# Kernel optimization log

Measured on AMD Instinct MI355X. Metric: run time of the kernel, lower is better.

## Reference

```python
import jax, jax.numpy as jnp
import numpy as np

NU, NI, D, E = 50000, 100000, 128, 500000
UMAX, IMAX = 50, 50
SQRT_D = float(np.sqrt(D))


def seg_softmax(vals, seg, n):
    # numerically stable softmax over edges grouped by segment id (sparse row softmax)
    m = jax.ops.segment_max(vals, seg, num_segments=n)
    ex = jnp.exp(vals - m[seg])
    s = jax.ops.segment_sum(ex, seg, num_segments=n)
    return ex / s[seg]


def setup_inputs() -> dict:
    key = jax.random.key(0)
    ks = jax.random.split(key, 20)
    w = lambda k: jax.random.normal(k, (D, D), dtype=jnp.float32) * 0.05
    return {
        "u_emb": jax.random.normal(ks[0], (NU, D), dtype=jnp.float32),
        "i_emb": jax.random.normal(ks[1], (NI, D), dtype=jnp.float32),
        "edge_u": jax.random.randint(ks[2], (E,), 0, NU),
        "edge_i": jax.random.randint(ks[3], (E,), 0, NI),
        "rui": jax.random.randint(ks[4], (E,), 0, UMAX),
        "riu": jax.random.randint(ks[5], (E,), 0, IMAX),
        "last_u_items": jax.random.randint(ks[6], (NU,), 0, NI),
        "last_i_users": jax.random.randint(ks[7], (NU,), 0, NU),
        "W1": w(ks[8]), "W2": w(ks[9]), "W1b": w(ks[10]), "W2b": w(ks[11]),
        "W3": w(ks[12]), "W4": w(ks[13]),
        "pV": jax.random.normal(ks[14], (UMAX, D), dtype=jnp.float32),
        "pK": jax.random.normal(ks[15], (IMAX, D), dtype=jnp.float32),
        "last_user_table": jax.random.normal(ks[16], (NU, D), dtype=jnp.float32),
        "last_item_table": jax.random.normal(ks[17], (NI, D), dtype=jnp.float32),
    }


def reference(u_emb, i_emb, edge_u, edge_i, rui, riu, last_u_items, last_i_users,
              W1, W2, W1b, W2b, W3, W4, pV, pK, last_user_table, last_item_table):
    # nn.Linear: y = x @ W.T
    um = u_emb @ W2.T            # (NU, D) user messages
    im = i_emb @ W1.T            # (NI, D) item messages
    um_e = um[edge_u]            # (E, D) gathered per edge
    im_e = im[edge_i]            # (E, D)

    # ---- long term ----
    # dense e = um @ im.T masked to edges == per-edge dot products (same math)
    e_vals = jnp.sum(um_e * im_e, axis=-1)                     # (E,)
    pVui = pV[rui]                                             # (E, D)
    pKiu = pK[riu]                                             # (E, D)
    e_ui = e_vals + jnp.sum(um_e * pVui, axis=-1)
    e_iu = e_vals + jnp.sum(im_e * pKiu, axis=-1)
    alphas = seg_softmax(e_ui / SQRT_D, edge_u, NU)            # softmax over items per user
    betas = seg_softmax(e_iu / SQRT_D, edge_i, NI)             # softmax over users per item

    umb = u_emb @ W2b.T
    imb = i_emb @ W1b.T
    # pass_messages: out[row] = sum_e alpha_e * (messages[col_e] + p_e)
    hLu = jax.ops.segment_sum(alphas[:, None] * (imb[edge_i] + pKiu), edge_u, num_segments=NU)
    hLi = jax.ops.segment_sum(betas[:, None] * (umb[edge_u] + pVui), edge_i, num_segments=NI)

    # ---- short term ----
    li = last_item_table[last_u_items] @ W3.T                  # (NU, D)
    lu = last_user_table[last_i_users] @ W4.T                  # (NU, D)
    a_vals = jnp.sum(li[edge_u] * im_e, axis=-1)               # (E,)
    b_vals = jnp.sum(lu[edge_u] * im_e, axis=-1)               # (E,)
    alphas_s = seg_softmax(a_vals / SQRT_D, edge_u, NU)
    betas_s = seg_softmax(b_vals / SQRT_D, edge_i, NI)
    # p = ones -> messages + 1
    hSu = jax.ops.segment_sum(alphas_s[:, None] * (im_e + 1.0), edge_u, num_segments=NU)
    hSi = jax.ops.segment_sum(betas_s[:, None] * (um_e + 1.0), edge_i, num_segments=NI)

    return (hLu, hSu, hLi, hSi)
```

## Files before the change

kernel.cpp:

```cpp
#include <hip/hip_runtime.h>
#include <hip/hip_bf16.h>
#include <math.h>

#define D_ 128
#define INV_SQRT_D 0.08838834764831845f
#define SCAN_CH 16
#define SCAN_TILE (256 * SCAN_CH)

typedef __bf16 bf16x8 __attribute__((ext_vector_type(8)));
typedef __bf16 bf16x4 __attribute__((ext_vector_type(4)));
typedef float f32x4 __attribute__((ext_vector_type(4)));

struct W6 { const float* p[6]; };

__device__ __forceinline__ void unpack8(bf16x8 v, float* f) {
    const uint32_t* u = (const uint32_t*)&v;
#pragma unroll
    for (int i = 0; i < 4; i++) {
        uint32_t w = u[i];
        f[2 * i]     = __uint_as_float(w << 16);
        f[2 * i + 1] = __uint_as_float(w & 0xffff0000u);
    }
}

__device__ __forceinline__ void unpack4(bf16x4 v, float* f) {
    const uint32_t* u = (const uint32_t*)&v;
#pragma unroll
    for (int i = 0; i < 2; i++) {
        uint32_t w = u[i];
        f[2 * i]     = __uint_as_float(w << 16);
        f[2 * i + 1] = __uint_as_float(w & 0xffff0000u);
    }
}

__global__ __launch_bounds__(256) void cvt_weights(W6 w, __bf16* __restrict__ out) {
    int idx = blockIdx.x * 256 + threadIdx.x;
    if (idx >= 6 * 16384) return;
    out[idx] = (__bf16)w.p[idx >> 14][idx & 16383];
}

__global__ __launch_bounds__(256) void cvt2(const float* __restrict__ a, const float* __restrict__ b,
                                            __bf16* __restrict__ oa, __bf16* __restrict__ ob, int n) {
    int idx = blockIdx.x * 256 + threadIdx.x;
    if (idx < n) { oa[idx] = (__bf16)a[idx]; ob[idx] = (__bf16)b[idx]; }
}

__global__ __launch_bounds__(256) void gemm_xwt(const float* __restrict__ X,
                                                const int* __restrict__ gidx,
                                                const __bf16* __restrict__ Wb,
                                                __bf16* __restrict__ Y, int rows) {
    int lane = threadIdx.x & 63;
    int wave = threadIdx.x >> 6;
    int row0 = blockIdx.x * 64 + wave * 16;
    if (row0 >= rows) return;
    int l16 = lane & 15, kh = lane >> 4;
    int ar = row0 + l16;
    int arc = ar < rows ? ar : rows - 1;
    long srcrow = gidx ? (long)gidx[arc] : (long)arc;
    const float* arow = X + (size_t)srcrow * D_;

    f32x4 acc[8] = {};
#pragma unroll
    for (int k0 = 0; k0 < D_; k0 += 32) {
        int kk = k0 + kh * 8;
        float4 a0 = *(const float4*)(arow + kk);
        float4 a1 = *(const float4*)(arow + kk + 4);
        bf16x8 af;
        af[0] = (__bf16)a0.x; af[1] = (__bf16)a0.y; af[2] = (__bf16)a0.z; af[3] = (__bf16)a0.w;
        af[4] = (__bf16)a1.x; af[5] = (__bf16)a1.y; af[6] = (__bf16)a1.z; af[7] = (__bf16)a1.w;
#pragma unroll
        for (int cb = 0; cb < 8; cb++) {
            bf16x8 bf = *(const bf16x8*)(Wb + (size_t)(cb * 16 + l16) * D_ + kk);
            acc[cb] = __builtin_amdgcn_mfma_f32_16x16x32_bf16(af, bf, acc[cb], 0, 0, 0);
        }
    }
#pragma unroll
    for (int cb = 0; cb < 8; cb++) {
#pragma unroll
        for (int j = 0; j < 4; j++) {
            int r = row0 + kh * 4 + j;
            if (r < rows) Y[(size_t)r * D_ + cb * 16 + l16] = (__bf16)acc[cb][j];
        }
    }
}

__global__ __launch_bounds__(256) void gemm_dual(const float* __restrict__ X,
                                                 const __bf16* __restrict__ WA,
                                                 const __bf16* __restrict__ WB,
                                                 __bf16* __restrict__ YA,
                                                 __bf16* __restrict__ YB, int rows) {
    int lane = threadIdx.x & 63;
    int wave = threadIdx.x >> 6;
    int row0 = blockIdx.x * 64 + wave * 16;
    if (row0 >= rows) return;
    int l16 = lane & 15, kh = lane >> 4;
    int ar = row0 + l16;
    int arc = ar < rows ? ar : rows - 1;
    const float* arow = X + (size_t)arc * D_;

    f32x4 accA[8] = {}, accB[8] = {};
#pragma unroll
    for (int k0 = 0; k0 < D_; k0 += 32) {
        int kk = k0 + kh * 8;
        float4 a0 = *(const float4*)(arow + kk);
        float4 a1 = *(const float4*)(arow + kk + 4);
        bf16x8 af;
        af[0] = (__bf16)a0.x; af[1] = (__bf16)a0.y; af[2] = (__bf16)a0.z; af[3] = (__bf16)a0.w;
        af[4] = (__bf16)a1.x; af[5] = (__bf16)a1.y; af[6] = (__bf16)a1.z; af[7] = (__bf16)a1.w;
#pragma unroll
        for (int cb = 0; cb < 8; cb++) {
            bf16x8 bfA = *(const bf16x8*)(WA + (size_t)(cb * 16 + l16) * D_ + kk);
            accA[cb] = __builtin_amdgcn_mfma_f32_16x16x32_bf16(af, bfA, accA[cb], 0, 0, 0);
            bf16x8 bfB = *(const bf16x8*)(WB + (size_t)(cb * 16 + l16) * D_ + kk);
            accB[cb] = __builtin_amdgcn_mfma_f32_16x16x32_bf16(af, bfB, accB[cb], 0, 0, 0);
        }
    }
#pragma unroll
    for (int cb = 0; cb < 8; cb++) {
#pragma unroll
        for (int j = 0; j < 4; j++) {
            int r = row0 + kh * 4 + j;
            if (r < rows) {
                YA[(size_t)r * D_ + cb * 16 + l16] = (__bf16)accA[cb][j];
                YB[(size_t)r * D_ + cb * 16 + l16] = (__bf16)accB[cb][j];
            }
        }
    }
}

__global__ __launch_bounds__(256) void gemm_pvk(const __bf16* __restrict__ Xb,
                                                const __bf16* __restrict__ Pb,
                                                float* __restrict__ Y, int rows, int ncols) {
    int lane = threadIdx.x & 63;
    int wave = threadIdx.x >> 6;
    int row0 = blockIdx.x * 64 + wave * 16;
    if (row0 >= rows) return;
    int l16 = lane & 15, kh = lane >> 4;
    int ar = row0 + l16;
    int arc = ar < rows ? ar : rows - 1;
    const __bf16* arow = Xb + (size_t)arc * D_;

    f32x4 acc[4] = {};
#pragma unroll
    for (int k0 = 0; k0 < D_; k0 += 32) {
        int kk = k0 + kh * 8;
        bf16x8 af = *(const bf16x8*)(arow + kk);
#pragma unroll
        for (int cb = 0; cb < 4; cb++) {
            int br = cb * 16 + l16;
            if (br >= ncols) br = ncols - 1;
            bf16x8 bf = *(const bf16x8*)(Pb + (size_t)br * D_ + kk);
            acc[cb] = __builtin_amdgcn_mfma_f32_16x16x32_bf16(af, bf, acc[cb], 0, 0, 0);
        }
    }
#pragma unroll
    for (int cb = 0; cb < 4; cb++) {
        int col = cb * 16 + l16;
        if (col >= ncols) continue;
#pragma unroll
        for (int j = 0; j < 4; j++) {
            int r = row0 + kh * 4 + j;
            if (r < rows) Y[(size_t)r * ncols + col] = acc[cb][j];
        }
    }
}

__global__ __launch_bounds__(256) void hist2(const int* __restrict__ eu, const int* __restrict__ ei,
                                             int* __restrict__ cnt_all, int nu, int E) {
    int e = blockIdx.x * 256 + threadIdx.x;
    if (e < E) {
        atomicAdd(&cnt_all[eu[e]], 1);
        atomicAdd(&cnt_all[nu + ei[e]], 1);
    }
}

__global__ __launch_bounds__(256) void scan_phaseA(const int* __restrict__ cnt, int* __restrict__ part, int n) {
    __shared__ int wsum[4];
    int t = threadIdx.x, lane = t & 63, w = t >> 6;
    int i0 = blockIdx.x * SCAN_TILE + t * SCAN_CH;
    int tot = 0;
#pragma unroll
    for (int j = 0; j < SCAN_CH; j++) tot += (i0 + j < n) ? cnt[i0 + j] : 0;
#pragma unroll
    for (int d = 32; d; d >>= 1) tot += __shfl_xor(tot, d);
    if (lane == 0) wsum[w] = tot;
    __syncthreads();
    if (t == 0) part[blockIdx.x] = wsum[0] + wsum[1] + wsum[2] + wsum[3];
}

__global__ __launch_bounds__(1024) void scan_phaseB(int* __restrict__ part, int nb,
                                                    int* __restrict__ off, int n) {
    __shared__ int wsum[16];
    int t = threadIdx.x, lane = t & 63, w = t >> 6;
    int v = (t < nb) ? part[t] : 0;
    int x = v;
#pragma unroll
    for (int d = 1; d < 64; d <<= 1) {
        int y = __shfl_up(x, d);
        if (lane >= d) x += y;
    }
    if (lane == 63) wsum[w] = x;
    __syncthreads();
    int wbase = 0;
    for (int ww = 0; ww < w; ww++) wbase += wsum[ww];
    if (t < nb) part[t] = wbase + x - v;
    if (t == 1023) off[n] = wbase + x;
}

__global__ __launch_bounds__(256) void scan_phaseC(const int* __restrict__ cnt, const int* __restrict__ part,
                                                   int* __restrict__ off, int* __restrict__ pos, int n) {
    __shared__ int wsum[4];
    int t = threadIdx.x, lane = t & 63, w = t >> 6;
    int i0 = blockIdx.x * SCAN_TILE + t * SCAN_CH;
    int loc[SCAN_CH];
    int tot = 0;
#pragma unroll
    for (int j = 0; j < SCAN_CH; j++) {
        int v = (i0 + j < n) ? cnt[i0 + j] : 0;
        loc[j] = tot; tot += v;
    }
    int x = tot;
#pragma unroll
    for (int d = 1; d < 64; d <<= 1) {
        int y = __shfl_up(x, d);
        if (lane >= d) x += y;
    }
    if (lane == 63) wsum[w] = x;
    __syncthreads();
    int wbase = 0;
    for (int ww = 0; ww < w; ww++) wbase += wsum[ww];
    int excl = part[blockIdx.x] + wbase + x - tot;
#pragma unroll
    for (int j = 0; j < SCAN_CH; j++) {
        if (i0 + j < n) { off[i0 + j] = excl + loc[j]; pos[i0 + j] = excl + loc[j]; }
    }
}

__global__ __launch_bounds__(256) void scatter2(const int* __restrict__ eu, const int* __restrict__ ei,
                                                int* __restrict__ pos_all, int* __restrict__ list_all,
                                                int nu, int E) {
    int e = blockIdx.x * 256 + threadIdx.x;
    if (e < E) {
        int pu = atomicAdd(&pos_all[eu[e]], 1);
        list_all[pu] = e;
        int pi = atomicAdd(&pos_all[nu + ei[e]], 1);
        list_all[pi] = e;
    }
}

__global__ __launch_bounds__(256) void edge_dots16(const __bf16* __restrict__ um, const __bf16* __restrict__ im,
                                                   const __bf16* __restrict__ li, const __bf16* __restrict__ lu,
                                                   const float* __restrict__ upv, const float* __restrict__ ipk,
                                                   const int* __restrict__ eu, const int* __restrict__ ei,
                                                   const int* __restrict__ rui, const int* __restrict__ riu,
                                                   float* __restrict__ e_ui, float* __restrict__ e_iu,
                                                   float* __restrict__ a_log, float* __restrict__ b_log,
                                                   int E, int umax, int imax) {
    int wave = threadIdx.x >> 6;
    int lane = threadIdx.x & 63;
    int g = lane >> 4, l16 = lane & 15;
    int e = blockIdx.x * 16 + wave * 4 + g;
    if (e >= E) return;
    int u = eu[e], it = ei[e];
    bf16x8 umv = ((const bf16x8*)(um + (size_t)u * D_))[l16];
    bf16x8 imv = ((const bf16x8*)(im + (size_t)it * D_))[l16];
    bf16x8 liv = ((const bf16x8*)(li + (size_t)u * D_))[l16];
    bf16x8 luv = ((const bf16x8*)(lu + (size_t)u * D_))[l16];
    float fu[8], fi[8], fl[8], fg[8];
    unpack8(umv, fu); unpack8(imv, fi); unpack8(liv, fl); unpack8(luv, fg);
    float s_mm = 0.f, s_li = 0.f, s_lu = 0.f;
#pragma unroll
    for (int j = 0; j < 8; j++) {
        s_mm = fmaf(fu[j], fi[j], s_mm);
        s_li = fmaf(fl[j], fi[j], s_li);
        s_lu = fmaf(fg[j], fi[j], s_lu);
    }
#pragma unroll
    for (int d = 1; d < 16; d <<= 1) {
        s_mm += __shfl_xor(s_mm, d);
        s_li += __shfl_xor(s_li, d);
        s_lu += __shfl_xor(s_lu, d);
    }
    if (l16 == 0) {
        float uv = upv[(size_t)u * umax + rui[e]];
        float iv = ipk[(size_t)it * imax + riu[e]];
        e_ui[e]  = (s_mm + uv) * INV_SQRT_D;
        e_iu[e]  = (s_mm + iv) * INV_SQRT_D;
        a_log[e] = s_li * INV_SQRT_D;
        b_log[e] = s_lu * INV_SQRT_D;
    }
}

__global__ __launch_bounds__(256) void user_messages(const int* __restrict__ off_all, const int* __restrict__ list_all,
                                                     const int* __restrict__ ei, const int* __restrict__ riu,
                                                     const float* __restrict__ e_ui, const float* __restrict__ a_log,
                                                     const __bf16* __restrict__ imb, const __bf16* __restrict__ im,
                                                     const __bf16* __restrict__ pKb,
                                                     float* __restrict__ hLu, float* __restrict__ hSu, int nu) {
    int u = blockIdx.x * 4 + (threadIdx.x >> 6);
    if (u >= nu) return;
    int lane = threadIdx.x & 63;
    int g = lane >> 5, l32 = lane & 31;
    int off = off_all[u], n = off_all[u + 1] - off;
    float a1[4] = {}, a2[4] = {};
    float s1 = 0.f, s2 = 0.f;
    float m1 = -INFINITY, m2 = -INFINITY;
    for (int i = lane; i < n; i += 64) {
        int e = list_all[off + i];
        m1 = fmaxf(m1, e_ui[e]);
        m2 = fmaxf(m2, a_log[e]);
    }
#pragma unroll
    for (int d = 32; d; d >>= 1) {
        m1 = fmaxf(m1, __shfl_xor(m1, d));
        m2 = fmaxf(m2, __shfl_xor(m2, d));
    }
    for (int i = g; i < n; i += 2) {
        int e = list_all[off + i];
        float w1 = __expf(e_ui[e] - m1);
        float w2 = __expf(a_log[e] - m2);
        int item = ei[e];
        bf16x4 vb = ((const bf16x4*)(imb + (size_t)item * D_))[l32];
        bf16x4 vi = ((const bf16x4*)(im + (size_t)item * D_))[l32];
        bf16x4 pk = ((const bf16x4*)(pKb + (size_t)riu[e] * D_))[l32];
        float fb[4], fv[4], fp[4];
        unpack4(vb, fb); unpack4(vi, fv); unpack4(pk, fp);
        s1 += w1; s2 += w2;
#pragma unroll
        for (int j = 0; j < 4; j++) {
            a1[j] = fmaf(w1, fb[j] + fp[j], a1[j]);
            a2[j] = fmaf(w2, fv[j] + 1.f, a2[j]);
        }
    }
#pragma unroll
    for (int j = 0; j < 4; j++) {
        a1[j] += __shfl_xor(a1[j], 32);
        a2[j] += __shfl_xor(a2[j], 32);
    }
    s1 += __shfl_xor(s1, 32);
    s2 += __shfl_xor(s2, 32);
    float inv1 = n > 0 ? 1.f / s1 : 0.f;
    float inv2 = n > 0 ? 1.f / s2 : 0.f;
    if (lane < 32) {
        float4 o1 = make_float4(a1[0] * inv1, a1[1] * inv1, a1[2] * inv1, a1[3] * inv1);
        float4 o2 = make_float4(a2[0] * inv2, a2[1] * inv2, a2[2] * inv2, a2[3] * inv2);
        ((float4*)(hLu + (size_t)u * D_))[lane] = o1;
        ((float4*)(hSu + (size_t)u * D_))[lane] = o2;
    }
}

__global__ __launch_bounds__(256) void item_messages(const int* __restrict__ off_all, const int* __restrict__ list_all,
                                                     const int* __restrict__ eu, const int* __restrict__ rui,
                                                     const float* __restrict__ e_iu, const float* __restrict__ b_log,
                                                     const __bf16* __restrict__ umb, const __bf16* __restrict__ um,
                                                     const __bf16* __restrict__ pVb,
                                                     float* __restrict__ hLi, float* __restrict__ hSi,
                                                     int nu, int ni) {
    int it = blockIdx.x * 4 + (threadIdx.x >> 6);
    if (it >= ni) return;
    int lane = threadIdx.x & 63;
    int g = lane >> 5, l32 = lane & 31;
    int off = off_all[nu + it], n = off_all[nu + it + 1] - off;
    float a1[4] = {}, a2[4] = {};
    float s1 = 0.f, s2 = 0.f;
    float m1 = -INFINITY, m2 = -INFINITY;
    for (int i = lane; i < n; i += 64) {
        int e = list_all[off + i];
        m1 = fmaxf(m1, e_iu[e]);
        m2 = fmaxf(m2, b_log[e]);
    }
#pragma unroll
    for (int d = 32; d; d >>= 1) {
        m1 = fmaxf(m1, __shfl_xor(m1, d));
        m2 = fmaxf(m2, __shfl_xor(m2, d));
    }
    for (int i = g; i < n; i += 2) {
        int e = list_all[off + i];
        float w1 = __expf(e_iu[e] - m1);
        float w2 = __expf(b_log[e] - m2);
        int user = eu[e];
        bf16x4 vb = ((const bf16x4*)(umb + (size_t)user * D_))[l32];
        bf16x4 vu = ((const bf16x4*)(um + (size_t)user * D_))[l32];
        bf16x4 pv = ((const bf16x4*)(pVb + (size_t)rui[e] * D_))[l32];
        float fb[4], fv[4], fp[4];
        unpack4(vb, fb); unpack4(vu, fv); unpack4(pv, fp);
        s1 += w1; s2 += w2;
#pragma unroll
        for (int j = 0; j < 4; j++) {
            a1[j] = fmaf(w1, fb[j] + fp[j], a1[j]);
            a2[j] = fmaf(w2, fv[j] + 1.f, a2[j]);
        }
    }
#pragma unroll
    for (int j = 0; j < 4; j++) {
        a1[j] += __shfl_xor(a1[j], 32);
        a2[j] += __shfl_xor(a2[j], 32);
    }
    s1 += __shfl_xor(s1, 32);
    s2 += __shfl_xor(s2, 32);
    float inv1 = n > 0 ? 1.f / s1 : 0.f;
    float inv2 = n > 0 ? 1.f / s2 : 0.f;
    if (lane < 32) {
        float4 o1 = make_float4(a1[0] * inv1, a1[1] * inv1, a1[2] * inv1, a1[3] * inv1);
        float4 o2 = make_float4(a2[0] * inv2, a2[1] * inv2, a2[2] * inv2, a2[3] * inv2);
        ((float4*)(hLi + (size_t)it * D_))[lane] = o1;
        ((float4*)(hSi + (size_t)it * D_))[lane] = o2;
    }
}

extern "C" void kernel_launch(void* const* d_in, const int* in_sizes, int n_in,
                              void* d_out, int out_size, void* d_ws, size_t ws_size,
                              hipStream_t stream) {
    (void)n_in; (void)out_size; (void)ws_size;
    const float* u_emb = (const float*)d_in[0];
    const float* i_emb = (const float*)d_in[1];
    const int* edge_u = (const int*)d_in[2];
    const int* edge_i = (const int*)d_in[3];
    const int* rui = (const int*)d_in[4];
    const int* riu = (const int*)d_in[5];
    const int* last_u_items = (const int*)d_in[6];
    const int* last_i_users = (const int*)d_in[7];
    const float* W1  = (const float*)d_in[8];
    const float* W2  = (const float*)d_in[9];
    const float* W1b = (const float*)d_in[10];
    const float* W2b = (const float*)d_in[11];
    const float* W3  = (const float*)d_in[12];
    const float* W4  = (const float*)d_in[13];
    const float* pV  = (const float*)d_in[14];
    const float* pK  = (const float*)d_in[15];
    const float* last_user_table = (const float*)d_in[16];
    const float* last_item_table = (const float*)d_in[17];

    const int NU = in_sizes[0] / D_;
    const int NI = in_sizes[1] / D_;
    const int E  = in_sizes[2];
    const int UMAXr = in_sizes[14] / D_;
    const int IMAXr = in_sizes[15] / D_;
    const int NSEG = NU + NI;

    size_t cur = 0;
    auto alloc = [&](size_t bytes) -> void* {
        void* p = (char*)d_ws + cur;
        cur += (bytes + 255) & ~(size_t)255;
        return p;
    };

    __bf16* Wb     = (__bf16*)alloc(6 * 16384 * sizeof(__bf16));
    __bf16* pVb    = (__bf16*)alloc((size_t)UMAXr * D_ * 2);
    __bf16* pKb    = (__bf16*)alloc((size_t)IMAXr * D_ * 2);
    __bf16* um_bf  = (__bf16*)alloc((size_t)NU * D_ * 2);
    __bf16* umb_bf = (__bf16*)alloc((size_t)NU * D_ * 2);
    __bf16* li_bf  = (__bf16*)alloc((size_t)NU * D_ * 2);
    __bf16* lu_bf  = (__bf16*)alloc((size_t)NU * D_ * 2);
    __bf16* im_bf  = (__bf16*)alloc((size_t)NI * D_ * 2);
    __bf16* imb_bf = (__bf16*)alloc((size_t)NI * D_ * 2);
    float* upv   = (float*)alloc((size_t)NU * UMAXr * 4);
    float* ipk   = (float*)alloc((size_t)NI * IMAXr * 4);
    float* e_ui  = (float*)alloc((size_t)E * 4);
    float* e_iu  = (float*)alloc((size_t)E * 4);
    float* a_log = (float*)alloc((size_t)E * 4);
    float* b_log = (float*)alloc((size_t)E * 4);
    int* cnt_all  = (int*)alloc((size_t)NSEG * 4);
    int* off_all  = (int*)alloc((size_t)(NSEG + 1) * 4);
    int* pos_all  = (int*)alloc((size_t)NSEG * 4);
    int* list_all = (int*)alloc((size_t)2 * E * 4);
    int* parts    = (int*)alloc(1024 * 4);

    float* out = (float*)d_out;
    float* hLu = out;
    float* hSu = out + (size_t)NU * D_;
    float* hLi = out + (size_t)2 * NU * D_;
    float* hSi = out + (size_t)2 * NU * D_ + (size_t)NI * D_;

    W6 w6;
    w6.p[0] = W1; w6.p[1] = W2; w6.p[2] = W1b; w6.p[3] = W2b; w6.p[4] = W3; w6.p[5] = W4;
    cvt_weights<<<(6 * 16384 + 255) / 256, 256, 0, stream>>>(w6, Wb);
    cvt2<<<(UMAXr * D_ + 255) / 256, 256, 0, stream>>>(pV, pK, pVb, pKb, UMAXr * D_);

    hipMemsetAsync(cnt_all, 0, (size_t)NSEG * 4, stream);
    hist2<<<(E + 255) / 256, 256, 0, stream>>>(edge_u, edge_i, cnt_all, NU, E);
    int nb = (NSEG + SCAN_TILE - 1) / SCAN_TILE;
    scan_phaseA<<<nb, 256, 0, stream>>>(cnt_all, parts, NSEG);
    scan_phaseB<<<1, 1024, 0, stream>>>(parts, nb, off_all, NSEG);
    scan_phaseC<<<nb, 256, 0, stream>>>(cnt_all, parts, off_all, pos_all, NSEG);
    scatter2<<<(E + 255) / 256, 256, 0, stream>>>(edge_u, edge_i, pos_all, list_all, NU, E);

    int gu = (NU + 63) / 64, gi = (NI + 63) / 64;
    gemm_dual<<<gi, 256, 0, stream>>>(i_emb, Wb + 0 * 16384, Wb + 2 * 16384, im_bf, imb_bf, NI);
    gemm_dual<<<gu, 256, 0, stream>>>(u_emb, Wb + 1 * 16384, Wb + 3 * 16384, um_bf, umb_bf, NU);
    gemm_xwt<<<gu, 256, 0, stream>>>(last_item_table, last_u_items, Wb + 4 * 16384, li_bf, NU);
    gemm_xwt<<<gu, 256, 0, stream>>>(last_user_table, last_i_users, Wb + 5 * 16384, lu_bf, NU);

    gemm_pvk<<<gu, 256, 0, stream>>>(um_bf, pVb, upv, NU, UMAXr);
    gemm_pvk<<<gi, 256, 0, stream>>>(im_bf, pKb, ipk, NI, IMAXr);

    edge_dots16<<<(E + 15) / 16, 256, 0, stream>>>(um_bf, im_bf, li_bf, lu_bf, upv, ipk,
                                                   edge_u, edge_i, rui, riu,
                                                   e_ui, e_iu, a_log, b_log, E, UMAXr, IMAXr);

    user_messages<<<(NU + 3) / 4, 256, 0, stream>>>(off_all, list_all, edge_i, riu, e_ui, a_log,
                                                    imb_bf, im_bf, pKb, hLu, hSu, NU);
    item_messages<<<(NI + 3) / 4, 256, 0, stream>>>(off_all, list_all, edge_u, rui, e_iu, b_log,
                                                    umb_bf, um_bf, pVb, hLi, hSi, NU, NI);
}
```

Baseline: 576.9 us.

## Fuse edge logits into segment kernels with online softmax and interleaved row records

Removes the separate per-edge dot-product kernel and its four E-sized logit arrays. The user and item aggregation kernels now compute the logits themselves and use an online (running-max) softmax in a single pass over each segment. Projected embeddings are stored interleaved per row (im|imb, um|umb|lu), so the gathers for one edge hit contiguous memory. The cost is that each edge's dot products are recomputed on both the user side and the item side, plus extra exp and rescale work per edge in the online softmax.

```diff
diff --git a/kernel.cpp b/kernel.cpp
--- a/kernel.cpp
+++ b/kernel.cpp
@@ -13,16 +13,6 @@
 
 struct W6 { const float* p[6]; };
 
-__device__ __forceinline__ void unpack8(bf16x8 v, float* f) {
-    const uint32_t* u = (const uint32_t*)&v;
-#pragma unroll
-    for (int i = 0; i < 4; i++) {
-        uint32_t w = u[i];
-        f[2 * i]     = __uint_as_float(w << 16);
-        f[2 * i + 1] = __uint_as_float(w & 0xffff0000u);
-    }
-}
-
 __device__ __forceinline__ void unpack4(bf16x4 v, float* f) {
     const uint32_t* u = (const uint32_t*)&v;
 #pragma unroll
@@ -48,7 +38,7 @@
 __global__ __launch_bounds__(256) void gemm_xwt(const float* __restrict__ X,
                                                 const int* __restrict__ gidx,
                                                 const __bf16* __restrict__ Wb,
-                                                __bf16* __restrict__ Y, int rows) {
+                                                __bf16* __restrict__ Y, int ystride, int rows) {
     int lane = threadIdx.x & 63;
     int wave = threadIdx.x >> 6;
     int row0 = blockIdx.x * 64 + wave * 16;
@@ -79,7 +69,7 @@
 #pragma unroll
         for (int j = 0; j < 4; j++) {
             int r = row0 + kh * 4 + j;
-            if (r < rows) Y[(size_t)r * D_ + cb * 16 + l16] = (__bf16)acc[cb][j];
+            if (r < rows) Y[(size_t)r * ystride + cb * 16 + l16] = (__bf16)acc[cb][j];
         }
     }
 }
@@ -87,8 +77,8 @@
 __global__ __launch_bounds__(256) void gemm_dual(const float* __restrict__ X,
                                                  const __bf16* __restrict__ WA,
                                                  const __bf16* __restrict__ WB,
-                                                 __bf16* __restrict__ YA,
-                                                 __bf16* __restrict__ YB, int rows) {
+                                                 __bf16* __restrict__ YA, int sA,
+                                                 __bf16* __restrict__ YB, int sB, int rows) {
     int lane = threadIdx.x & 63;
     int wave = threadIdx.x >> 6;
     int row0 = blockIdx.x * 64 + wave * 16;
@@ -121,14 +111,14 @@
         for (int j = 0; j < 4; j++) {
             int r = row0 + kh * 4 + j;
             if (r < rows) {
-                YA[(size_t)r * D_ + cb * 16 + l16] = (__bf16)accA[cb][j];
-                YB[(size_t)r * D_ + cb * 16 + l16] = (__bf16)accB[cb][j];
+                YA[(size_t)r * sA + cb * 16 + l16] = (__bf16)accA[cb][j];
+                YB[(size_t)r * sB + cb * 16 + l16] = (__bf16)accB[cb][j];
             }
         }
     }
 }
 
-__global__ __launch_bounds__(256) void gemm_pvk(const __bf16* __restrict__ Xb,
+__global__ __launch_bounds__(256) void gemm_pvk(const __bf16* __restrict__ Xb, int xstride,
                                                 const __bf16* __restrict__ Pb,
                                                 float* __restrict__ Y, int rows, int ncols) {
     int lane = threadIdx.x & 63;
@@ -138,7 +128,7 @@
     int l16 = lane & 15, kh = lane >> 4;
     int ar = row0 + l16;
     int arc = ar < rows ? ar : rows - 1;
-    const __bf16* arow = Xb + (size_t)arc * D_;
+    const __bf16* arow = Xb + (size_t)arc * xstride;
 
     f32x4 acc[4] = {};
 #pragma unroll
@@ -248,163 +238,184 @@
     }
 }
 
-__global__ __launch_bounds__(256) void edge_dots16(const __bf16* __restrict__ um, const __bf16* __restrict__ im,
-                                                   const __bf16* __restrict__ li, const __bf16* __restrict__ lu,
-                                                   const float* __restrict__ upv, const float* __restrict__ ipk,
-                                                   const int* __restrict__ eu, const int* __restrict__ ei,
-                                                   const int* __restrict__ rui, const int* __restrict__ riu,
-                                                   float* __restrict__ e_ui, float* __restrict__ e_iu,
-                                                   float* __restrict__ a_log, float* __restrict__ b_log,
-                                                   int E, int umax, int imax) {
-    int wave = threadIdx.x >> 6;
-    int lane = threadIdx.x & 63;
-    int g = lane >> 4, l16 = lane & 15;
-    int e = blockIdx.x * 16 + wave * 4 + g;
-    if (e >= E) return;
-    int u = eu[e], it = ei[e];
-    bf16x8 umv = ((const bf16x8*)(um + (size_t)u * D_))[l16];
-    bf16x8 imv = ((const bf16x8*)(im + (size_t)it * D_))[l16];
-    bf16x8 liv = ((const bf16x8*)(li + (size_t)u * D_))[l16];
-    bf16x8 luv = ((const bf16x8*)(lu + (size_t)u * D_))[l16];
-    float fu[8], fi[8], fl[8], fg[8];
-    unpack8(umv, fu); unpack8(imv, fi); unpack8(liv, fl); unpack8(luv, fg);
-    float s_mm = 0.f, s_li = 0.f, s_lu = 0.f;
-#pragma unroll
-    for (int j = 0; j < 8; j++) {
-        s_mm = fmaf(fu[j], fi[j], s_mm);
-        s_li = fmaf(fl[j], fi[j], s_li);
-        s_lu = fmaf(fg[j], fi[j], s_lu);
-    }
-#pragma unroll
-    for (int d = 1; d < 16; d <<= 1) {
-        s_mm += __shfl_xor(s_mm, d);
-        s_li += __shfl_xor(s_li, d);
-        s_lu += __shfl_xor(s_lu, d);
-    }
-    if (l16 == 0) {
-        float uv = upv[(size_t)u * umax + rui[e]];
-        float iv = ipk[(size_t)it * imax + riu[e]];
-        e_ui[e]  = (s_mm + uv) * INV_SQRT_D;
-        e_iu[e]  = (s_mm + iv) * INV_SQRT_D;
-        a_log[e] = s_li * INV_SQRT_D;
-        b_log[e] = s_lu * INV_SQRT_D;
-    }
-}
-
-__global__ __launch_bounds__(256) void user_messages(const int* __restrict__ off_all, const int* __restrict__ list_all,
-                                                     const int* __restrict__ ei, const int* __restrict__ riu,
-                                                     const float* __restrict__ e_ui, const float* __restrict__ a_log,
-                                                     const __bf16* __restrict__ imb, const __bf16* __restrict__ im,
-                                                     const __bf16* __restrict__ pKb,
-                                                     float* __restrict__ hLu, float* __restrict__ hSu, int nu) {
+__global__ __launch_bounds__(256) void user_fused(const int* __restrict__ off_all, const int* __restrict__ list_all,
+                                                  const int* __restrict__ ei, const int* __restrict__ rui,
+                                                  const int* __restrict__ riu,
+                                                  const __bf16* __restrict__ i_rec,
+                                                  const __bf16* __restrict__ u_rec,
+                                                  const __bf16* __restrict__ li,
+                                                  const __bf16* __restrict__ pKb,
+                                                  const float* __restrict__ upv,
+                                                  float* __restrict__ hLu, float* __restrict__ hSu,
+                                                  int nu, int umax) {
     int u = blockIdx.x * 4 + (threadIdx.x >> 6);
     if (u >= nu) return;
     int lane = threadIdx.x & 63;
     int g = lane >> 5, l32 = lane & 31;
     int off = off_all[u], n = off_all[u + 1] - off;
-    float a1[4] = {}, a2[4] = {};
-    float s1 = 0.f, s2 = 0.f;
-    float m1 = -INFINITY, m2 = -INFINITY;
-    for (int i = lane; i < n; i += 64) {
-        int e = list_all[off + i];
-        m1 = fmaxf(m1, e_ui[e]);
-        m2 = fmaxf(m2, a_log[e]);
-    }
-#pragma unroll
-    for (int d = 32; d; d >>= 1) {
-        m1 = fmaxf(m1, __shfl_xor(m1, d));
-        m2 = fmaxf(m2, __shfl_xor(m2, d));
-    }
+    if (n == 0) {
+        if (lane < 32) {
+            ((float4*)(hLu + (size_t)u * D_))[l32] = make_float4(0.f, 0.f, 0.f, 0.f);
+            ((float4*)(hSu + (size_t)u * D_))[l32] = make_float4(0.f, 0.f, 0.f, 0.f);
+        }
+        return;
+    }
+    float um4[4], li4[4];
+    unpack4(*(const bf16x4*)(u_rec + (size_t)u * 384 + l32 * 4), um4);
+    unpack4(*(const bf16x4*)(li + (size_t)u * D_ + l32 * 4), li4);
+    const float* upv_row = upv + (size_t)u * umax;
+
+    float m1 = -INFINITY, s1 = 0.f, a1[4] = {};
+    float m2 = -INFINITY, s2 = 0.f, a2[4] = {};
     for (int i = g; i < n; i += 2) {
         int e = list_all[off + i];
-        float w1 = __expf(e_ui[e] - m1);
-        float w2 = __expf(a_log[e] - m2);
         int item = ei[e];
-        bf16x4 vb = ((const bf16x4*)(imb + (size_t)item * D_))[l32];
-        bf16x4 vi = ((const bf16x4*)(im + (size_t)item * D_))[l32];
-        bf16x4 pk = ((const bf16x4*)(pKb + (size_t)riu[e] * D_))[l32];
-        float fb[4], fv[4], fp[4];
-        unpack4(vb, fb); unpack4(vi, fv); unpack4(pk, fp);
-        s1 += w1; s2 += w2;
+        const __bf16* ib = i_rec + (size_t)item * 256;
+        bf16x4 imv  = ((const bf16x4*)ib)[l32];
+        bf16x4 imbv = ((const bf16x4*)(ib + 128))[l32];
+        bf16x4 pkv  = ((const bf16x4*)(pKb + (size_t)riu[e] * D_))[l32];
+        float uv = upv_row[rui[e]];
+        float fim[4], fimb[4], fpk[4];
+        unpack4(imv, fim); unpack4(imbv, fimb); unpack4(pkv, fpk);
+        float d1 = 0.f, d2 = 0.f;
 #pragma unroll
         for (int j = 0; j < 4; j++) {
-            a1[j] = fmaf(w1, fb[j] + fp[j], a1[j]);
-            a2[j] = fmaf(w2, fv[j] + 1.f, a2[j]);
-        }
-    }
-#pragma unroll
-    for (int j = 0; j < 4; j++) {
-        a1[j] += __shfl_xor(a1[j], 32);
-        a2[j] += __shfl_xor(a2[j], 32);
-    }
+            d1 = fmaf(um4[j], fim[j], d1);
+            d2 = fmaf(li4[j], fim[j], d2);
+        }
+#pragma unroll
+        for (int d = 16; d; d >>= 1) {
+            d1 += __shfl_xor(d1, d);
+            d2 += __shfl_xor(d2, d);
+        }
+        float lg1 = (d1 + uv) * INV_SQRT_D;
+        float lg2 = d2 * INV_SQRT_D;
+        float mn = fmaxf(m1, lg1);
+        float r  = __expf(m1 - mn);
+        float w  = __expf(lg1 - mn);
+        s1 = s1 * r + w; m1 = mn;
+#pragma unroll
+        for (int j = 0; j < 4; j++) a1[j] = fmaf(a1[j], r, w * (fimb[j] + fpk[j]));
+        mn = fmaxf(m2, lg2);
+        r  = __expf(m2 - mn);
+        w  = __expf(lg2 - mn);
+        s2 = s2 * r + w; m2 = mn;
+#pragma unroll
+        for (int j = 0; j < 4; j++) a2[j] = fmaf(a2[j], r, w * (fim[j] + 1.f));
+    }
+    float mo = __shfl_xor(m1, 32);
+    float mm = fmaxf(m1, mo);
+    float r  = __expf(m1 - mm);
+    s1 *= r;
+#pragma unroll
+    for (int j = 0; j < 4; j++) a1[j] *= r;
     s1 += __shfl_xor(s1, 32);
+#pragma unroll
+    for (int j = 0; j < 4; j++) a1[j] += __shfl_xor(a1[j], 32);
+    mo = __shfl_xor(m2, 32);
+    mm = fmaxf(m2, mo);
+    r  = __expf(m2 - mm);
+    s2 *= r;
+#pragma unroll
+    for (int j = 0; j < 4; j++) a2[j] *= r;
     s2 += __shfl_xor(s2, 32);
-    float inv1 = n > 0 ? 1.f / s1 : 0.f;
-    float inv2 = n > 0 ? 1.f / s2 : 0.f;
+#pragma unroll
+    for (int j = 0; j < 4; j++) a2[j] += __shfl_xor(a2[j], 32);
+
+    float inv1 = 1.f / s1, inv2 = 1.f / s2;
     if (lane < 32) {
-        float4 o1 = make_float4(a1[0] * inv1, a1[1] * inv1, a1[2] * inv1, a1[3] * inv1);
-        float4 o2 = make_float4(a2[0] * inv2, a2[1] * inv2, a2[2] * inv2, a2[3] * inv2);
-        ((float4*)(hLu + (size_t)u * D_))[lane] = o1;
-        ((float4*)(hSu + (size_t)u * D_))[lane] = o2;
-    }
-}
-
-__global__ __launch_bounds__(256) void item_messages(const int* __restrict__ off_all, const int* __restrict__ list_all,
-                                                     const int* __restrict__ eu, const int* __restrict__ rui,
-                                                     const float* __restrict__ e_iu, const float* __restrict__ b_log,
-                                                     const __bf16* __restrict__ umb, const __bf16* __restrict__ um,
-                                                     const __bf16* __restrict__ pVb,
-                                                     float* __restrict__ hLi, float* __restrict__ hSi,
-                                                     int nu, int ni) {
+        ((float4*)(hLu + (size_t)u * D_))[l32] = make_float4(a1[0] * inv1, a1[1] * inv1, a1[2] * inv1, a1[3] * inv1);
+        ((float4*)(hSu + (size_t)u * D_))[l32] = make_float4(a2[0] * inv2, a2[1] * inv2, a2[2] * inv2, a2[3] * inv2);
+    }
+}
+
+__global__ __launch_bounds__(256) void item_fused(const int* __restrict__ off_all, const int* __restrict__ list_all,
+                                                  const int* __restrict__ eu, const int* __restrict__ rui,
+                                                  const int* __restrict__ riu,
+                                                  const __bf16* __restrict__ i_rec,
+                                                  const __bf16* __restrict__ u_rec,
+                                                  const __bf16* __restrict__ pVb,
+                                                  const float* __restrict__ ipk,
+                                                  float* __restrict__ hLi, float* __restrict__ hSi,
+                                                  int nu, int ni, int imax) {
     int it = blockIdx.x * 4 + (threadIdx.x >> 6);
     if (it >= ni) return;
     int lane = threadIdx.x & 63;
     int g = lane >> 5, l32 = lane & 31;
     int off = off_all[nu + it], n = off_all[nu + it + 1] - off;
-    float a1[4] = {}, a2[4] = {};
-    float s1 = 0.f, s2 = 0.f;
-    float m1 = -INFINITY, m2 = -INFINITY;
-    for (int i = lane; i < n; i += 64) {
-        int e = list_all[off + i];
-        m1 = fmaxf(m1, e_iu[e]);
-        m2 = fmaxf(m2, b_log[e]);
-    }
-#pragma unroll
-    for (int d = 32; d; d >>= 1) {
-        m1 = fmaxf(m1, __shfl_xor(m1, d));
-        m2 = fmaxf(m2, __shfl_xor(m2, d));
-    }
+    if (n == 0) {
+        if (lane < 32) {
+            ((float4*)(hLi + (size_t)it * D_))[l32] = make_float4(0.f, 0.f, 0.f, 0.f);
+            ((float4*)(hSi + (size_t)it * D_))[l32] = make_float4(0.f, 0.f, 0.f, 0.f);
+        }
+        return;
+    }
+    float im4[4];
+    unpack4(*(const bf16x4*)(i_rec + (size_t)it * 256 + l32 * 4), im4);
+    const float* ipk_row = ipk + (size_t)it * imax;
+
+    float m1 = -INFINITY, s1 = 0.f, a1[4] = {};
+    float m2 = -INFINITY, s2 = 0.f, a2[4] = {};
     for (int i = g; i < n; i += 2) {
         int e = list_all[off + i];
-        float w1 = __expf(e_iu[e] - m1);
-        float w2 = __expf(b_log[e] - m2);
         int user = eu[e];
-        bf16x4 vb = ((const bf16x4*)(umb + (size_t)user * D_))[l32];
-        bf16x4 vu = ((const bf16x4*)(um + (size_t)user * D_))[l32];
-        bf16x4 pv = ((const bf16x4*)(pVb + (size_t)rui[e] * D_))[l32];
-        float fb[4], fv[4], fp[4];
-        unpack4(vb, fb); unpack4(vu, fv); unpack4(pv, fp);
-        s1 += w1; s2 += w2;
+        const __bf16* ub = u_rec + (size_t)user * 384;
+        bf16x4 umv  = ((const bf16x4*)ub)[l32];
+        bf16x4 umbv = ((const bf16x4*)(ub + 128))[l32];
+        bf16x4 luv  = ((const bf16x4*)(ub + 256))[l32];
+        bf16x4 pvv  = ((const bf16x4*)(pVb + (size_t)rui[e] * D_))[l32];
+        float iv = ipk_row[riu[e]];
+        float fum[4], fumb[4], flu[4], fpv[4];
+        unpack4(umv, fum); unpack4(umbv, fumb); unpack4(luv, flu); unpack4(pvv, fpv);
+        float d1 = 0.f, d2 = 0.f;
 #pragma unroll
         for (int j = 0; j < 4; j++) {
-            a1[j] = fmaf(w1, fb[j] + fp[j], a1[j]);
-            a2[j] = fmaf(w2, fv[j] + 1.f, a2[j]);
-        }
-    }
-#pragma unroll
-    for (int j = 0; j < 4; j++) {
-        a1[j] += __shfl_xor(a1[j], 32);
-        a2[j] += __shfl_xor(a2[j], 32);
-    }
+            d1 = fmaf(fum[j], im4[j], d1);
+            d2 = fmaf(flu[j], im4[j], d2);
+        }
+#pragma unroll
+        for (int d = 16; d; d >>= 1) {
+            d1 += __shfl_xor(d1, d);
+            d2 += __shfl_xor(d2, d);
+        }
+        float lg1 = (d1 + iv) * INV_SQRT_D;
+        float lg2 = d2 * INV_SQRT_D;
+        float mn = fmaxf(m1, lg1);
+        float r  = __expf(m1 - mn);
+        float w  = __expf(lg1 - mn);
+        s1 = s1 * r + w; m1 = mn;
+#pragma unroll
+        for (int j = 0; j < 4; j++) a1[j] = fmaf(a1[j], r, w * (fumb[j] + fpv[j]));
+        mn = fmaxf(m2, lg2);
+        r  = __expf(m2 - mn);
+        w  = __expf(lg2 - mn);
+        s2 = s2 * r + w; m2 = mn;
+#pragma unroll
+        for (int j = 0; j < 4; j++) a2[j] = fmaf(a2[j], r, w * (fum[j] + 1.f));
+    }
+    float mo = __shfl_xor(m1, 32);
+    float mm = fmaxf(m1, mo);
+    float r  = __expf(m1 - mm);
+    s1 *= r;
+#pragma unroll
+    for (int j = 0; j < 4; j++) a1[j] *= r;
     s1 += __shfl_xor(s1, 32);
+#pragma unroll
+    for (int j = 0; j < 4; j++) a1[j] += __shfl_xor(a1[j], 32);
+    mo = __shfl_xor(m2, 32);
+    mm = fmaxf(m2, mo);
+    r  = __expf(m2 - mm);
+    s2 *= r;
+#pragma unroll
+    for (int j = 0; j < 4; j++) a2[j] *= r;
     s2 += __shfl_xor(s2, 32);
-    float inv1 = n > 0 ? 1.f / s1 : 0.f;
-    float inv2 = n > 0 ? 1.f / s2 : 0.f;
+#pragma unroll
+    for (int j = 0; j < 4; j++) a2[j] += __shfl_xor(a2[j], 32);
+
+    float inv1 = 1.f / s1, inv2 = 1.f / s2;
     if (lane < 32) {
-        float4 o1 = make_float4(a1[0] * inv1, a1[1] * inv1, a1[2] * inv1, a1[3] * inv1);
-        float4 o2 = make_float4(a2[0] * inv2, a2[1] * inv2, a2[2] * inv2, a2[3] * inv2);
-        ((float4*)(hLi + (size_t)it * D_))[lane] = o1;
-        ((float4*)(hSi + (size_t)it * D_))[lane] = o2;
+        ((float4*)(hLi + (size_t)it * D_))[l32] = make_float4(a1[0] * inv1, a1[1] * inv1, a1[2] * inv1, a1[3] * inv1);
+        ((float4*)(hSi + (size_t)it * D_))[l32] = make_float4(a2[0] * inv2, a2[1] * inv2, a2[2] * inv2, a2[3] * inv2);
     }
 }
 
@@ -445,21 +456,14 @@
         return p;
     };
 
-    __bf16* Wb     = (__bf16*)alloc(6 * 16384 * sizeof(__bf16));
-    __bf16* pVb    = (__bf16*)alloc((size_t)UMAXr * D_ * 2);
-    __bf16* pKb    = (__bf16*)alloc((size_t)IMAXr * D_ * 2);
-    __bf16* um_bf  = (__bf16*)alloc((size_t)NU * D_ * 2);
-    __bf16* umb_bf = (__bf16*)alloc((size_t)NU * D_ * 2);
-    __bf16* li_bf  = (__bf16*)alloc((size_t)NU * D_ * 2);
-    __bf16* lu_bf  = (__bf16*)alloc((size_t)NU * D_ * 2);
-    __bf16* im_bf  = (__bf16*)alloc((size_t)NI * D_ * 2);
-    __bf16* imb_bf = (__bf16*)alloc((size_t)NI * D_ * 2);
+    __bf16* Wb    = (__bf16*)alloc(6 * 16384 * sizeof(__bf16));
+    __bf16* pVb   = (__bf16*)alloc((size_t)UMAXr * D_ * 2);
+    __bf16* pKb   = (__bf16*)alloc((size_t)IMAXr * D_ * 2);
+    __bf16* i_rec = (__bf16*)alloc((size_t)NI * 256 * 2);
+    __bf16* u_rec = (__bf16*)alloc((size_t)NU * 384 * 2);
+    __bf16* li_bf = (__bf16*)alloc((size_t)NU * D_ * 2);
     float* upv   = (float*)alloc((size_t)NU * UMAXr * 4);
     float* ipk   = (float*)alloc((size_t)NI * IMAXr * 4);
-    float* e_ui  = (float*)alloc((size_t)E * 4);
-    float* e_iu  = (float*)alloc((size_t)E * 4);
-    float* a_log = (float*)alloc((size_t)E * 4);
-    float* b_log = (float*)alloc((size_t)E * 4);
     int* cnt_all  = (int*)alloc((size_t)NSEG * 4);
     int* off_all  = (int*)alloc((size_t)(NSEG + 1) * 4);
     int* pos_all  = (int*)alloc((size_t)NSEG * 4);
@@ -486,20 +490,18 @@
     scatter2<<<(E + 255) / 256, 256, 0, stream>>>(edge_u, edge_i, pos_all, list_all, NU, E);
 
     int gu = (NU + 63) / 64, gi = (NI + 63) / 64;
-    gemm_dual<<<gi, 256, 0, stream>>>(i_emb, Wb + 0 * 16384, Wb + 2 * 16384, im_bf, imb_bf, NI);
-    gemm_dual<<<gu, 256, 0, stream>>>(u_emb, Wb + 1 * 16384, Wb + 3 * 16384, um_bf, umb_bf, NU);
-    gemm_xwt<<<gu, 256, 0, stream>>>(last_item_table, last_u_items, Wb + 4 * 16384, li_bf, NU);
-    gemm_xwt<<<gu, 256, 0, stream>>>(last_user_table, last_i_users, Wb + 5 * 16384, lu_bf, NU);
-
-    gemm_pvk<<<gu, 256, 0, stream>>>(um_bf, pVb, upv, NU, UMAXr);
-    gemm_pvk<<<gi, 256, 0, stream>>>(im_bf, pKb, ipk, NI, IMAXr);
-
-    edge_dots16<<<(E + 15) / 16, 256, 0, stream>>>(um_bf, im_bf, li_bf, lu_bf, upv, ipk,
-                                                   edge_u, edge_i, rui, riu,
-                                                   e_ui, e_iu, a_log, b_log, E, UMAXr, IMAXr);
-
-    user_messages<<<(NU + 3) / 4, 256, 0, stream>>>(off_all, list_all, edge_i, riu, e_ui, a_log,
-                                                    imb_bf, im_bf, pKb, hLu, hSu, NU);
-    item_messages<<<(NI + 3) / 4, 256, 0, stream>>>(off_all, list_all, edge_u, rui, e_iu, b_log,
-                                                    umb_bf, um_bf, pVb, hLi, hSi, NU, NI);
-}
+    gemm_dual<<<gi, 256, 0, stream>>>(i_emb, Wb + 0 * 16384, Wb + 2 * 16384,
+                                      i_rec + 0, 256, i_rec + 128, 256, NI);
+    gemm_dual<<<gu, 256, 0, stream>>>(u_emb, Wb + 1 * 16384, Wb + 3 * 16384,
+                                      u_rec + 0, 384, u_rec + 128, 384, NU);
+    gemm_xwt<<<gu, 256, 0, stream>>>(last_item_table, last_u_items, Wb + 4 * 16384, li_bf, 128, NU);
+    gemm_xwt<<<gu, 256, 0, stream>>>(last_user_table, last_i_users, Wb + 5 * 16384, u_rec + 256, 384, NU);
+
+    gemm_pvk<<<gu, 256, 0, stream>>>(u_rec, 384, pVb, upv, NU, UMAXr);
+    gemm_pvk<<<gi, 256, 0, stream>>>(i_rec, 256, pKb, ipk, NI, IMAXr);
+
+    user_fused<<<(NU + 3) / 4, 256, 0, stream>>>(off_all, list_all, edge_i, rui, riu,
+                                                 i_rec, u_rec, li_bf, pKb, upv, hLu, hSu, NU, UMAXr);
+    item_fused<<<(NI + 3) / 4, 256, 0, stream>>>(off_all, list_all, edge_u, rui, riu,
+                                                 i_rec, u_rec, pVb, ipk, hLi, hSi, NU, NI, IMAXr);
+}
```

Result: faster. 497.7 us (-13.7%).
